# Performance work log

Hardware: AMD Instinct MI355X
Metric: run time of the kernel (lower is better)

The kernel has to match this reference:

```python
import jax, jax.numpy as jnp
import numpy as np

B, C, H, W = 4, 128, 128, 128
SPHERE_SIZE, NUM_VOTES, NUM_PTS = 32768, 32, 4096
HW = H * W


def setup_inputs() -> dict:
    key = jax.random.key(0)
    k1, k2, k3, k4 = jax.random.split(key, 4)
    x = jax.random.normal(k1, (B, C, H, W), dtype=jnp.float32)
    vote_index = jax.random.randint(k2, (SPHERE_SIZE, NUM_VOTES), 0, HW, dtype=jnp.int32)
    vote_weight = jax.random.uniform(k3, (SPHERE_SIZE, NUM_VOTES), dtype=jnp.float32)
    inds = jax.random.randint(k4, (B, NUM_PTS), 0, SPHERE_SIZE, dtype=jnp.int64)
    return {"x": x, "vote_index": vote_index, "vote_weight": vote_weight, "inds": inds}


def reference(x, vote_index, vote_weight, inds):
    b, c, h, w = x.shape
    xf = x.reshape(b, c, h * w)                      # [B, C, HW]
    idx = jnp.take(vote_index, inds, axis=0)          # [B, P, V] flat HT indices
    wts = jnp.take(vote_weight, inds, axis=0)         # [B, P, V] vote weights

    def per_batch(xb, ib, wb):
        # xb: [C, HW], ib/wb: [P, V]
        g = jnp.take(xb, ib, axis=1)                  # [C, P, V] gather
        return jnp.einsum('cpv,pv->cp', g, wb)        # weighted vote accumulation

    return jax.vmap(per_batch)(xf, idx, wts)          # [B, C, P]
```

## Files before the change

### kernel.cpp

```cpp
#include <hip/hip_runtime.h>

typedef _Float16 half_t;
typedef _Float16 half8_t __attribute__((ext_vector_type(8)));
typedef float    f32x4  __attribute__((ext_vector_type(4)));

constexpr int BB  = 4;
constexpr int CC  = 128;
constexpr int HWW = 16384;
constexpr int NV  = 32;
constexpr int NP  = 4096;
constexpr int PT  = 8;
constexpr int GT  = 128;

__global__ __launch_bounds__(256) void transpose_h(const float* __restrict__ x,
                                                   half_t* __restrict__ xt) {
  __shared__ float tile[64][65];
  const int b   = blockIdx.z;
  const int hw0 = blockIdx.x * 64;
  const int c0  = blockIdx.y * 64;
  const int tid = threadIdx.x;
  const float* xb = x + (size_t)b * CC * HWW;

  const int hw4 = (tid & 15) * 4;
  const int cr  = tid >> 4;
#pragma unroll
  for (int j = 0; j < 4; ++j) {
    const int c = cr + j * 16;
    const f32x4 v = __builtin_nontemporal_load(
        reinterpret_cast<const f32x4*>(xb + (size_t)(c0 + c) * HWW + hw0 + hw4));
    tile[c][hw4 + 0] = v.x;
    tile[c][hw4 + 1] = v.y;
    tile[c][hw4 + 2] = v.z;
    tile[c][hw4 + 3] = v.w;
  }
  __syncthreads();

  half_t* xtb = xt + (size_t)b * HWW * CC;
  const int c8 = (tid & 7) * 8;
  const int hr = tid >> 3;
#pragma unroll
  for (int j = 0; j < 2; ++j) {
    const int hwr = hr + j * 32;
    half8_t hv;
#pragma unroll
    for (int k = 0; k < 8; ++k) hv[k] = (half_t)tile[c8 + k][hwr];
    *reinterpret_cast<half8_t*>(xtb + (size_t)(hw0 + hwr) * CC + c0 + c8) = hv;
  }
}

__global__ __launch_bounds__(GT, 4) void gather_h(const half_t* __restrict__ xt,
                                                  const int* __restrict__ vote_index,
                                                  const float* __restrict__ vote_weight,
                                                  const int* __restrict__ inds,
                                                  float* __restrict__ out) {
  const int b   = blockIdx.y;
  const int p0  = blockIdx.x * PT;
  const int tid = threadIdx.x;
  const int sg  = tid >> 4;
  const int c8  = tid & 15;

  __shared__ int   s_idx[PT][NV];
  __shared__ float s_w[PT][NV];
#pragma unroll
  for (int i = tid; i < PT * NV; i += GT) {
    const int pp = i >> 5;
    const int v  = i & (NV - 1);
    const int s  = inds[b * NP + p0 + pp];
    s_idx[pp][v] = vote_index[s * NV + v] * CC;
    s_w[pp][v]   = vote_weight[s * NV + v];
  }
  __syncthreads();

  const half_t* xb = xt + (size_t)b * HWW * CC + c8 * 8;

  float acc[8] = {0.f, 0.f, 0.f, 0.f, 0.f, 0.f, 0.f, 0.f};
#pragma unroll
  for (int v = 0; v < NV; ++v) {
    const half8_t xv = *reinterpret_cast<const half8_t*>(xb + s_idx[sg][v]);
    const float   w  = s_w[sg][v];
#pragma unroll
    for (int k = 0; k < 8; ++k) acc[k] += (float)xv[k] * w;
  }
  __syncthreads();

  __shared__ float s_out[PT][CC + 4];
#pragma unroll
  for (int k = 0; k < 8; ++k) s_out[sg][c8 * 8 + k] = acc[k];
  __syncthreads();

  float* ob = out + ((size_t)b * CC + tid) * NP + p0;
  const f32x4 o0 = {s_out[0][tid], s_out[1][tid], s_out[2][tid], s_out[3][tid]};
  const f32x4 o1 = {s_out[4][tid], s_out[5][tid], s_out[6][tid], s_out[7][tid]};
  __builtin_nontemporal_store(o0, reinterpret_cast<f32x4*>(ob));
  __builtin_nontemporal_store(o1, reinterpret_cast<f32x4*>(ob + 4));
}

__global__ __launch_bounds__(128) void gather_fallback_k(const float* __restrict__ x,
                                                         const int* __restrict__ vote_index,
                                                         const float* __restrict__ vote_weight,
                                                         const int* __restrict__ inds,
                                                         float* __restrict__ out) {
  const int b = blockIdx.y;
  const int p = blockIdx.x;
  const int c = threadIdx.x;
  const int s = inds[b * NP + p];
  const float* xb = x + ((size_t)b * CC + c) * HWW;
  float a = 0.f;
  for (int v = 0; v < NV; ++v)
    a += xb[vote_index[s * NV + v]] * vote_weight[s * NV + v];
  out[((size_t)b * CC + c) * NP + p] = a;
}

extern "C" void kernel_launch(void* const* d_in, const int* in_sizes, int n_in,
                              void* d_out, int out_size, void* d_ws, size_t ws_size,
                              hipStream_t stream) {
  const float* x           = (const float*)d_in[0];
  const int*   vote_index  = (const int*)d_in[1];
  const float* vote_weight = (const float*)d_in[2];
  const int*   inds        = (const int*)d_in[3];
  float*       out         = (float*)d_out;

  const size_t xt_bytes = (size_t)BB * HWW * CC * sizeof(half_t);
  if (ws_size >= xt_bytes) {
    half_t* xt = (half_t*)d_ws;
    dim3 tg(HWW / 64, CC / 64, BB);
    transpose_h<<<tg, 256, 0, stream>>>(x, xt);
    dim3 gg(NP / PT, BB);
    gather_h<<<gg, GT, 0, stream>>>(xt, vote_index, vote_weight, inds, out);
  } else {
    dim3 gg(NP, BB);
    gather_fallback_k<<<gg, CC, 0, stream>>>(x, vote_index, vote_weight, inds, out);
  }
}
```

Baseline: 111.6 us.

## Split channels per block and interleave batches in flattened 1D grids

Gather blocks now cover 16 points and half the channels (64) instead of 8 points and all 128. Each thread therefore loads a 128-byte contiguous slice per vote, and each output row gets 64-byte contiguous stores. Both kernels move to 1D grids whose low block-id bits interleave batch and channel-half, so concurrently running blocks spread across batches. This changes cache locality and wave scheduling, and halves the bytes each gathered row contributes per block.

```diff
diff --git a/kernel.cpp b/kernel.cpp
--- a/kernel.cpp
+++ b/kernel.cpp
@@ -9,15 +9,17 @@
 constexpr int HWW = 16384;
 constexpr int NV  = 32;
 constexpr int NP  = 4096;
-constexpr int PT  = 8;
-constexpr int GT  = 128;
+constexpr int PT  = 16;
+
 
 __global__ __launch_bounds__(256) void transpose_h(const float* __restrict__ x,
                                                    half_t* __restrict__ xt) {
   __shared__ float tile[64][65];
-  const int b   = blockIdx.z;
-  const int hw0 = blockIdx.x * 64;
-  const int c0  = blockIdx.y * 64;
+  const int bid = blockIdx.x;
+  const int q   = bid & 7;
+  const int b   = q >> 1;
+  const int c0  = (q & 1) * 64;
+  const int hw0 = (bid >> 3) * 64;
   const int tid = threadIdx.x;
   const float* xb = x + (size_t)b * CC * HWW;
 
@@ -48,21 +50,24 @@
   }
 }
 
-__global__ __launch_bounds__(GT, 4) void gather_h(const half_t* __restrict__ xt,
-                                                  const int* __restrict__ vote_index,
-                                                  const float* __restrict__ vote_weight,
-                                                  const int* __restrict__ inds,
-                                                  float* __restrict__ out) {
-  const int b   = blockIdx.y;
-  const int p0  = blockIdx.x * PT;
+__global__ __launch_bounds__(128, 4) void gather_h(const half_t* __restrict__ xt,
+                                                   const int* __restrict__ vote_index,
+                                                   const float* __restrict__ vote_weight,
+                                                   const int* __restrict__ inds,
+                                                   float* __restrict__ out) {
+  const int bid = blockIdx.x;
+  const int q   = bid & 7;
+  const int b   = q >> 1;
+  const int h   = q & 1;
+  const int p0  = (bid >> 3) * PT;
   const int tid = threadIdx.x;
-  const int sg  = tid >> 4;
-  const int c8  = tid & 15;
+  const int sg  = tid >> 3;
+  const int c8  = tid & 7;
 
   __shared__ int   s_idx[PT][NV];
   __shared__ float s_w[PT][NV];
 #pragma unroll
-  for (int i = tid; i < PT * NV; i += GT) {
+  for (int i = tid; i < PT * NV; i += 128) {
     const int pp = i >> 5;
     const int v  = i & (NV - 1);
     const int s  = inds[b * NP + p0 + pp];
@@ -71,7 +76,7 @@
   }
   __syncthreads();
 
-  const half_t* xb = xt + (size_t)b * HWW * CC + c8 * 8;
+  const half_t* xb = xt + (size_t)b * HWW * CC + h * 64 + c8 * 8;
 
   float acc[8] = {0.f, 0.f, 0.f, 0.f, 0.f, 0.f, 0.f, 0.f};
 #pragma unroll
@@ -83,14 +88,18 @@
   }
   __syncthreads();
 
-  __shared__ float s_out[PT][CC + 4];
+  __shared__ float s_out[64][PT + 4];
 #pragma unroll
-  for (int k = 0; k < 8; ++k) s_out[sg][c8 * 8 + k] = acc[k];
+  for (int k = 0; k < 8; ++k) s_out[c8 * 8 + k][sg] = acc[k];
   __syncthreads();
 
-  float* ob = out + ((size_t)b * CC + tid) * NP + p0;
-  const f32x4 o0 = {s_out[0][tid], s_out[1][tid], s_out[2][tid], s_out[3][tid]};
-  const f32x4 o1 = {s_out[4][tid], s_out[5][tid], s_out[6][tid], s_out[7][tid]};
+  const int cloc = tid >> 1;
+  const int ph   = (tid & 1) * 8;
+  float* ob = out + ((size_t)b * CC + 64 * h + cloc) * NP + p0 + ph;
+  const f32x4 o0 = {s_out[cloc][ph + 0], s_out[cloc][ph + 1],
+                    s_out[cloc][ph + 2], s_out[cloc][ph + 3]};
+  const f32x4 o1 = {s_out[cloc][ph + 4], s_out[cloc][ph + 5],
+                    s_out[cloc][ph + 6], s_out[cloc][ph + 7]};
   __builtin_nontemporal_store(o0, reinterpret_cast<f32x4*>(ob));
   __builtin_nontemporal_store(o1, reinterpret_cast<f32x4*>(ob + 4));
 }
@@ -123,10 +132,8 @@
   const size_t xt_bytes = (size_t)BB * HWW * CC * sizeof(half_t);
   if (ws_size >= xt_bytes) {
     half_t* xt = (half_t*)d_ws;
-    dim3 tg(HWW / 64, CC / 64, BB);
-    transpose_h<<<tg, 256, 0, stream>>>(x, xt);
-    dim3 gg(NP / PT, BB);
-    gather_h<<<gg, GT, 0, stream>>>(xt, vote_index, vote_weight, inds, out);
+    transpose_h<<<2048, 256, 0, stream>>>(x, xt);
+    gather_h<<<2048, 128, 0, stream>>>(xt, vote_index, vote_weight, inds, out);
   } else {
     dim3 gg(NP, BB);
     gather_fallback_k<<<gg, CC, 0, stream>>>(x, vote_index, vote_weight, inds, out);
```

New measurement: 98.02 us. 12.2% less time.
